# Kernel tuning notes

Measured on AMD Instinct MI355X. Metric: run time of the kernel, lower is better.

The kernel has to match this reference:

```python
import jax, jax.numpy as jnp
import numpy as np
from jax import lax

R = 3                      # blob_r
S = 2 * R + 1              # 7: maxpool / neighborhood kernel size
THRESH = 0.997
PS_XY = 0.1                # vs_xy
PS_Z = 0.02                # vs_z
ZMIN = -2.0                # zrange[0]
K_PEAKS = 131072           # static upper bound replacing torch.nonzero

_offs = np.arange(S)
_gz, _gy, _gx = np.meshgrid(_offs, _offs, _offs, indexing='ij')  # patch axis order [z,y,x]
GZ = jnp.asarray(_gz.ravel(), dtype=jnp.int32)
GY = jnp.asarray(_gy.ravel(), dtype=jnp.int32)
GX = jnp.asarray(_gx.ravel(), dtype=jnp.int32)
# centroid filters: offsets -r..r along the matching patch axis (matches torch meshgrid layout)
FZ = jnp.asarray((_gz.ravel() - R).astype(np.float32))
FY = jnp.asarray((_gy.ravel() - R).astype(np.float32))
FX = jnp.asarray((_gx.ravel() - R).astype(np.float32))


def setup_inputs() -> dict:
    key = jax.random.key(0)
    pred_vol = jax.random.uniform(key, (1, 1, 128, 512, 512), dtype=jnp.float32)
    return {"pred_vol": pred_vol, "max_peaks": K_PEAKS}


def _forward(pred_vol, max_peaks):
    vol = pred_vol[0, 0]                               # [D,H,W]
    D, H, W = vol.shape
    thr = jnp.where(vol > THRESH, vol, 0.0)
    # MaxPool3d(kernel=2r+1, stride=1, padding=r) == SAME max window (pad with -inf)
    mp = lax.reduce_window(thr, -jnp.inf, lax.max, (S, S, S), (1, 1, 1), [(R, R)] * 3)
    conf = jnp.where((mp > 0.0) & (mp == thr), mp, 0.0)  # local maxima above threshold
    # fixed-size peak extraction (replaces torch.nonzero); zero-valued entries are padding
    vals, idx = lax.top_k(conf.reshape(-1), max_peaks)   # [K], [K]
    z = idx // (H * W)
    y = (idx % (H * W)) // W
    x = idx % W
    padv = jnp.pad(vol, R)                               # ConstantPad3d(r, 0)
    # gather (2r+1)^3 neighborhoods around each peak: [K, S^3]
    patches = padv[z[:, None] + GZ[None, :], y[:, None] + GY[None, :], x[:, None] + GX[None, :]]
    s0 = patches.sum(axis=1)                             # conv3d with ones filter == conf_rec sum
    xloc = jnp.einsum('kp,p->k', patches, FX) / s0
    yloc = jnp.einsum('kp,p->k', patches, FY) / s0
    zloc = jnp.einsum('kp,p->k', patches, FZ) / s0
    xf = x.astype(jnp.float32)
    yf = y.astype(jnp.float32)
    zf = z.astype(jnp.float32)
    xrec = (xf + xloc - (W - 1) / 2.0) * PS_XY
    yrec = (yf + yloc - (H - 1) / 2.0) * PS_XY
    zrec = (zf + zloc + 0.5) * PS_Z + ZMIN
    valid = vals > 0.0
    xyz = jnp.where(valid[:, None], jnp.stack((xrec, yrec, zrec), axis=1), 0.0)  # [K,3]
    out = jnp.concatenate([xyz, vals[:, None]], axis=1)  # [K,4] = (x,y,z,conf), padded rows are 0
    return out, valid


def reference(pred_vol, max_peaks):
    return _forward(pred_vol, max_peaks)
```

## Files before the change

### kernel.cpp

```cpp
#include <hip/hip_runtime.h>

#define DD 128
#define HH 512
#define WW 512
#define NVOX (DD*HH*WW)
#define THRESHV 0.997f
#define KPEAKS 131072
#define PEAK_CAP (1u<<18)
#define NBINS 65536


__global__ void k_init(unsigned* counters, unsigned* hist) {
    unsigned t = blockIdx.x * 1024u + threadIdx.x;
    if (t < 64) counters[t] = 0u;
    if (t < NBINS) hist[t] = 0u;
}

__global__ __launch_bounds__(256, 8)
void k_find(const float4* __restrict__ vol4, const float* __restrict__ vol,
            unsigned* counters, unsigned* hist,
            unsigned long long* keys, float4* psums) {
    __shared__ unsigned lcnt, pcnt, lbase;
    __shared__ unsigned cidx[384];
    __shared__ unsigned long long lbuf[192];
    __shared__ float4 sbuf[192];
    if (threadIdx.x == 0) { lcnt = 0; pcnt = 0; }
    __syncthreads();

    unsigned t = threadIdx.x;
    unsigned lane = t & 63u;
    unsigned w = t >> 6;
    unsigned base4 = blockIdx.x * 2048u;

    float4 v[8];
#pragma unroll
    for (unsigned i = 0; i < 8; i++) v[i] = vol4[base4 + i * 256u + t];
    unsigned m = 0u;
#pragma unroll
    for (unsigned i = 0; i < 8; i++) {
        m |= (v[i].x > THRESHV ? 1u : 0u) << (4 * i);
        m |= (v[i].y > THRESHV ? 1u : 0u) << (4 * i + 1);
        m |= (v[i].z > THRESHV ? 1u : 0u) << (4 * i + 2);
        m |= (v[i].w > THRESHV ? 1u : 0u) << (4 * i + 3);
    }
    while (m) {
        int b = __ffs(m) - 1;
        m &= m - 1u;
        unsigned f4 = base4 + ((unsigned)b >> 2) * 256u + t;
        cidx[atomicAdd(&lcnt, 1u) & 383u] = f4 * 4u + ((unsigned)b & 3u);
    }
    __syncthreads();

    unsigned n = lcnt > 384u ? 384u : lcnt;
    int dz = (int)lane / 7, dy = (int)lane - dz * 7;
    for (unsigned base = w * 2u; base < n; base += 8u) {
        bool has2 = (base + 1u < n);
        unsigned idxA = cidx[base];
        unsigned idxB = has2 ? cidx[base + 1u] : idxA;
        int zA = idxA >> 18, yA = (idxA >> 9) & 511, xA = idxA & 511;
        int zB = idxB >> 18, yB = (idxB >> 9) & 511, xB = idxB & 511;
        int nzA = zA + dz - 3, nyA = yA + dy - 3;
        int nzB = zB + dz - 3, nyB = yB + dy - 3;
        bool rowokA = (lane < 49) && ((unsigned)nzA < DD) && ((unsigned)nyA < HH);
        bool rowokB = (lane < 49) && ((unsigned)nzB < DD) && ((unsigned)nyB < HH);
        size_t rbA = rowokA ? (((size_t)(unsigned)nzA << 18) | ((size_t)(unsigned)nyA << 9))
                            : (((size_t)zA << 18) | ((size_t)yA << 9));
        size_t rbB = rowokB ? (((size_t)(unsigned)nzB << 18) | ((size_t)(unsigned)nyB << 9))
                            : (((size_t)zB << 18) | ((size_t)yB << 9));
        float rvA[7], rvB[7];
        bool intAB = (xA >= 3) && (xA <= WW - 4) && (xB >= 3) && (xB <= WW - 4);
        if (intAB) {
            float4 fA0 = *(const float4*)(vol + rbA + (unsigned)(xA - 3));
            float4 fA1 = *(const float4*)(vol + rbA + (unsigned)(xA + 1));
            float4 fB0 = *(const float4*)(vol + rbB + (unsigned)(xB - 3));
            float4 fB1 = *(const float4*)(vol + rbB + (unsigned)(xB + 1));
            rvA[0] = fA0.x; rvA[1] = fA0.y; rvA[2] = fA0.z; rvA[3] = fA0.w;
            rvA[4] = fA1.x; rvA[5] = fA1.y; rvA[6] = fA1.z;
            rvB[0] = fB0.x; rvB[1] = fB0.y; rvB[2] = fB0.z; rvB[3] = fB0.w;
            rvB[4] = fB1.x; rvB[5] = fB1.y; rvB[6] = fB1.z;
        } else {
#pragma unroll
            for (int d = 0; d < 7; d++) {
                int nxA = xA + d - 3;
                bool okA = (unsigned)nxA < WW;
                float va = vol[rbA + (unsigned)(okA ? nxA : xA)];
                rvA[d] = okA ? va : 0.f;
                int nxB = xB + d - 3;
                bool okB = (unsigned)nxB < WW;
                float vb = vol[rbB + (unsigned)(okB ? nxB : xB)];
                rvB[d] = okB ? vb : 0.f;
            }
        }
        if (!rowokA) {
#pragma unroll
            for (int d = 0; d < 7; d++) rvA[d] = 0.f;
        }
        if (!rowokB) {
#pragma unroll
            for (int d = 0; d < 7; d++) rvB[d] = 0.f;
        }
        float centerA = __shfl(rvA[3], 24);
        float centerB = __shfl(rvB[3], 24);

        {
            bool kill = false;
            float s0r = 0.f, sxr = 0.f;
#pragma unroll
            for (int d = 0; d < 7; d++) {
                kill |= rvA[d] > centerA;
                s0r += rvA[d];
                sxr += rvA[d] * (float)(d - 3);
            }
            if (!__any(kill)) {
                float s0 = s0r, sx = sxr;
                float sy = s0r * (float)(dy - 3);
                float sz = s0r * (float)(dz - 3);
                for (int off = 32; off; off >>= 1) {
                    s0 += __shfl_down(s0, off);
                    sx += __shfl_down(sx, off);
                    sy += __shfl_down(sy, off);
                    sz += __shfl_down(sz, off);
                }
                if (lane == 0) {
                    unsigned bits = __float_as_uint(centerA);
                    atomicAdd(&hist[(~bits) & 0xFFFFu], 1u);
                    unsigned li = atomicAdd(&pcnt, 1u);
                    if (li < 192u) {
                        lbuf[li] = ((unsigned long long)bits << 32) | idxA;
                        sbuf[li] = make_float4(s0, sx, sy, sz);
                    }
                }
            }
        }
        if (has2) {
            bool kill = false;
            float s0r = 0.f, sxr = 0.f;
#pragma unroll
            for (int d = 0; d < 7; d++) {
                kill |= rvB[d] > centerB;
                s0r += rvB[d];
                sxr += rvB[d] * (float)(d - 3);
            }
            if (!__any(kill)) {
                float s0 = s0r, sx = sxr;
                float sy = s0r * (float)(dy - 3);
                float sz = s0r * (float)(dz - 3);
                for (int off = 32; off; off >>= 1) {
                    s0 += __shfl_down(s0, off);
                    sx += __shfl_down(sx, off);
                    sy += __shfl_down(sy, off);
                    sz += __shfl_down(sz, off);
                }
                if (lane == 0) {
                    unsigned bits = __float_as_uint(centerB);
                    atomicAdd(&hist[(~bits) & 0xFFFFu], 1u);
                    unsigned li = atomicAdd(&pcnt, 1u);
                    if (li < 192u) {
                        lbuf[li] = ((unsigned long long)bits << 32) | idxB;
                        sbuf[li] = make_float4(s0, sx, sy, sz);
                    }
                }
            }
        }
    }
    __syncthreads();
    if (threadIdx.x == 0) lbase = atomicAdd(&counters[1], pcnt);
    __syncthreads();
    unsigned np = pcnt > 192u ? 192u : pcnt;
    for (unsigned i = threadIdx.x; i < np; i += 256u) {
        unsigned p = lbase + i;
        if (p < PEAK_CAP) { keys[p] = lbuf[i]; psums[p] = sbuf[i]; }
    }
}

__global__ void k_scan(const unsigned* __restrict__ hist, unsigned* cursor) {
    __shared__ unsigned partial[1024];
    int t = threadIdx.x;
    const uint4* h4 = (const uint4*)(hist + t * 64);
    uint4 loc[16];
#pragma unroll
    for (int i = 0; i < 16; i++) loc[i] = h4[i];
    unsigned s = 0;
#pragma unroll
    for (int i = 0; i < 16; i++) s += loc[i].x + loc[i].y + loc[i].z + loc[i].w;
    partial[t] = s;
    __syncthreads();
    for (int off = 1; off < 1024; off <<= 1) {
        unsigned v = (t >= off) ? partial[t - off] : 0u;
        __syncthreads();
        partial[t] += v;
        __syncthreads();
    }
    unsigned run = (t == 0) ? 0u : partial[t - 1];
    uint4* c4 = (uint4*)(cursor + t * 64);
#pragma unroll
    for (int i = 0; i < 16; i++) {
        uint4 h = loc[i]; uint4 o;
        o.x = run; run += h.x;
        o.y = run; run += h.y;
        o.z = run; run += h.z;
        o.w = run; run += h.w;
        c4[i] = o;
    }
}

__global__ void k_scatter(const unsigned* __restrict__ counters,
                          const unsigned long long* __restrict__ keys,
                          unsigned* cursor, unsigned long long* sorted,
                          unsigned* sslot,
                          float4* __restrict__ out, float* __restrict__ valid) {
    unsigned np = counters[1]; if (np > PEAK_CAP) np = PEAK_CAP;
    unsigned t = blockIdx.x * 1024u + threadIdx.x;
    if (t < np) {
        unsigned long long key = keys[t];
        unsigned bits = (unsigned)(key >> 32);
        unsigned pos = atomicAdd(&cursor[(~bits) & 0xFFFFu], 1u);
        if (pos < PEAK_CAP) { sorted[pos] = key; sslot[pos] = t; }
    } else if (t < KPEAKS) {
        out[t] = make_float4(0.f, 0.f, 0.f, 0.f);
        valid[t] = 0.f;
    }
}

__global__ void k_finish(const unsigned* __restrict__ counters,
                         const unsigned long long* __restrict__ sorted,
                         const unsigned* __restrict__ sslot,
                         const float4* __restrict__ psums,
                         float4* __restrict__ out, float* __restrict__ valid) {
    unsigned np = counters[1]; if (np > PEAK_CAP) np = PEAK_CAP;
    unsigned t = blockIdx.x * 1024u + threadIdx.x;
    if (t >= np) return;
    unsigned long long key = sorted[t];
    unsigned bits = (unsigned)(key >> 32);
    unsigned s = t;
    while (s > 0 && (unsigned)(sorted[s - 1] >> 32) == bits) s--;
    unsigned myidx = (unsigned)key;
    unsigned rank = 0, e = s;
    while (e < np) {
        unsigned long long k2 = sorted[e];
        if ((unsigned)(k2 >> 32) != bits) break;
        if ((unsigned)k2 < myidx) rank++;
        e++;
    }
    unsigned row = s + rank;
    if (row >= KPEAKS) return;
    unsigned idx = myidx;
    int z = idx >> 18, y = (idx >> 9) & 511, x = idx & 511;
    float4 ps = psums[sslot[t]];
    float val = __uint_as_float(bits);
    float xloc = ps.y / ps.x, yloc = ps.z / ps.x, zloc = ps.w / ps.x;
    float xr = ((float)x + xloc - (float)(WW - 1) * 0.5f) * 0.1f;
    float yr = ((float)y + yloc - (float)(HH - 1) * 0.5f) * 0.1f;
    float zr = ((float)z + zloc + 0.5f) * 0.02f - 2.0f;
    out[row] = make_float4(xr, yr, zr, val);
    valid[row] = 1.f;
}

extern "C" void kernel_launch(void* const* d_in, const int* in_sizes, int n_in,
                              void* d_out, int out_size, void* d_ws, size_t ws_size,
                              hipStream_t stream) {
    const float* vol = (const float*)d_in[0];

    char* w = (char*)d_ws;
    unsigned* counters = (unsigned*)w;
    unsigned* hist     = (unsigned*)(w + 1024);
    unsigned* cursor   = (unsigned*)(w + 1024 + NBINS * 4);
    char* w2 = w + 1024 + 2 * NBINS * 4;
    unsigned long long* keys   = (unsigned long long*)w2;
    unsigned long long* sorted = keys + PEAK_CAP;
    unsigned* sslot = (unsigned*)(sorted + PEAK_CAP);
    float4*   psums = (float4*)(sslot + PEAK_CAP);

    float* out_rows = (float*)d_out;
    float* valid = out_rows + (size_t)KPEAKS * 4;

    k_init<<<NBINS / 1024, 1024, 0, stream>>>(counters, hist);
    k_find<<<NVOX / 8192, 256, 0, stream>>>((const float4*)vol, vol, counters, hist, keys, psums);
    k_scan<<<1, 1024, 0, stream>>>(hist, cursor);
    k_scatter<<<PEAK_CAP / 1024, 1024, 0, stream>>>(counters, keys, cursor, sorted, sslot,
                                                    (float4*)out_rows, valid);
    k_finish<<<PEAK_CAP / 1024, 1024, 0, stream>>>(counters, sorted, sslot, psums,
                                                   (float4*)out_rows, valid);
}
```

Baseline: 264.0 us.

## Split peak finding into streaming threshold pass and separate neighborhood verify pass

The fused find kernel is split in two. A streaming kernel only thresholds the volume and compacts candidate voxel indices into a global list. A separate verify kernel, launched with a fixed grid, does the 7x7x7 local-max check and the neighborhood sums over that compacted list. The goal is to keep the bandwidth-bound streaming pass free of the irregular gather work that stalled blocks with many candidates, and to spread verification evenly across waves. The cost is an extra kernel launch and a global round trip for the candidates, which reuse the sorted buffer and counters[0].

Measured after the change: 324.1 us. +22.8%, slower.

```diff
diff --git a/kernel.cpp b/kernel.cpp
--- a/kernel.cpp
+++ b/kernel.cpp
@@ -7,6 +7,7 @@
 #define THRESHV 0.997f
 #define KPEAKS 131072
 #define PEAK_CAP (1u<<18)
+#define CAND_CAP (1u<<18)
 #define NBINS 65536
 
 
@@ -17,24 +18,20 @@
 }
 
 __global__ __launch_bounds__(256, 8)
-void k_find(const float4* __restrict__ vol4, const float* __restrict__ vol,
-            unsigned* counters, unsigned* hist,
-            unsigned long long* keys, float4* psums) {
-    __shared__ unsigned lcnt, pcnt, lbase;
+void k_stream(const float4* __restrict__ vol4, unsigned* counters,
+              unsigned* __restrict__ cand) {
+    __shared__ unsigned lcnt, lbase;
     __shared__ unsigned cidx[384];
-    __shared__ unsigned long long lbuf[192];
-    __shared__ float4 sbuf[192];
-    if (threadIdx.x == 0) { lcnt = 0; pcnt = 0; }
+    if (threadIdx.x == 0) lcnt = 0;
     __syncthreads();
 
     unsigned t = threadIdx.x;
-    unsigned lane = t & 63u;
-    unsigned w = t >> 6;
     unsigned base4 = blockIdx.x * 2048u;
 
     float4 v[8];
 #pragma unroll
     for (unsigned i = 0; i < 8; i++) v[i] = vol4[base4 + i * 256u + t];
+    __builtin_amdgcn_sched_barrier(0);
     unsigned m = 0u;
 #pragma unroll
     for (unsigned i = 0; i < 8; i++) {
@@ -50,13 +47,36 @@
         cidx[atomicAdd(&lcnt, 1u) & 383u] = f4 * 4u + ((unsigned)b & 3u);
     }
     __syncthreads();
-
     unsigned n = lcnt > 384u ? 384u : lcnt;
+    if (threadIdx.x == 0) lbase = atomicAdd(&counters[0], n);
+    __syncthreads();
+    for (unsigned i = t; i < n; i += 256u) {
+        unsigned p = lbase + i;
+        if (p < CAND_CAP) cand[p] = cidx[i];
+    }
+}
+
+__global__ __launch_bounds__(256, 8)
+void k_verify(const float* __restrict__ vol, const unsigned* __restrict__ cand,
+              unsigned* counters, unsigned* hist,
+              unsigned long long* keys, float4* psums) {
+    __shared__ unsigned pcnt, lbase;
+    __shared__ unsigned long long lbuf[192];
+    __shared__ float4 sbuf[192];
+    if (threadIdx.x == 0) pcnt = 0;
+    __syncthreads();
+
+    unsigned t = threadIdx.x;
+    unsigned lane = t & 63u;
+    unsigned w = t >> 6;
+    unsigned nc = counters[0]; if (nc > CAND_CAP) nc = CAND_CAP;
+    unsigned gw = blockIdx.x * 4u + w;
     int dz = (int)lane / 7, dy = (int)lane - dz * 7;
-    for (unsigned base = w * 2u; base < n; base += 8u) {
-        bool has2 = (base + 1u < n);
-        unsigned idxA = cidx[base];
-        unsigned idxB = has2 ? cidx[base + 1u] : idxA;
+
+    for (unsigned base = gw * 2u; base < nc; base += 16384u) {
+        bool has2 = (base + 1u < nc);
+        unsigned idxA = cand[base];
+        unsigned idxB = has2 ? cand[base + 1u] : idxA;
         int zA = idxA >> 18, yA = (idxA >> 9) & 511, xA = idxA & 511;
         int zB = idxB >> 18, yB = (idxB >> 9) & 511, xB = idxB & 511;
         int nzA = zA + dz - 3, nyA = yA + dy - 3;
@@ -271,11 +291,14 @@
     unsigned* sslot = (unsigned*)(sorted + PEAK_CAP);
     float4*   psums = (float4*)(sslot + PEAK_CAP);
 
+    unsigned* cand = (unsigned*)sorted;
+
     float* out_rows = (float*)d_out;
     float* valid = out_rows + (size_t)KPEAKS * 4;
 
     k_init<<<NBINS / 1024, 1024, 0, stream>>>(counters, hist);
-    k_find<<<NVOX / 8192, 256, 0, stream>>>((const float4*)vol, vol, counters, hist, keys, psums);
+    k_stream<<<NVOX / 8192, 256, 0, stream>>>((const float4*)vol, counters, cand);
+    k_verify<<<2048, 256, 0, stream>>>(vol, cand, counters, hist, keys, psums);
     k_scan<<<1, 1024, 0, stream>>>(hist, cursor);
     k_scatter<<<PEAK_CAP / 1024, 1024, 0, stream>>>(counters, keys, cursor, sorted, sslot,
                                                     (float4*)out_rows, valid);
```
